# Performance work log

Hardware: AMD Instinct MI355X
Metric: run time of the kernel (lower is better)

## Reference

```python
import jax, jax.numpy as jnp
import numpy as np

N = 100000   # nodes
E = 1600000  # edges (avg degree 16)
G = 64       # graphs in the batch


def setup_inputs() -> dict:
    key = jax.random.key(0)
    ks = jax.random.split(key, 12)
    x = jax.random.normal(ks[0], (N, 1), jnp.float32)
    src = jax.random.randint(ks[1], (E,), 0, N)
    dst = jax.random.randint(ks[2], (E,), 0, N)
    batch = jnp.sort(jax.random.randint(ks[3], (N,), 0, G))
    def glorot(k, shape):
        fan_in, fan_out = shape
        lim = (6.0 / (fan_in + fan_out)) ** 0.5
        return jax.random.uniform(k, shape, jnp.float32, -lim, lim)
    return {
        "x": x, "src": src, "dst": dst, "batch": batch,
        "W1": glorot(ks[4], (1, 100)),   "b1": jnp.zeros((100,), jnp.float32),
        "W2": glorot(ks[5], (100, 200)), "b2": jnp.zeros((200,), jnp.float32),
        "Wl1": glorot(ks[6], (200, 100)), "bl1": jnp.zeros((100,), jnp.float32),
        "Wl2": glorot(ks[7], (100, 1)),   "bl2": jnp.zeros((1,), jnp.float32),
    }


def gcn_layer(x, W, b, src, dst, n_nodes):
    """PyG GCNConv: linear, then sym-normalized aggregation with self-loops, then bias."""
    h = x @ W                                   # [N, out]
    deg = jax.ops.segment_sum(jnp.ones_like(src, dtype=h.dtype), dst,
                              num_segments=n_nodes) + 1.0  # +1 for self-loop
    dinv = jax.lax.rsqrt(deg)                   # [N]
    norm = dinv[src] * dinv[dst]                # [E]
    agg = jax.ops.segment_sum(h[src] * norm[:, None], dst, num_segments=n_nodes)
    agg = agg + h * (dinv * dinv)[:, None]      # self-loop message
    return agg + b


def reference(x, src, dst, batch, W1, b1, W2, b2, Wl1, bl1, Wl2, bl2):
    n = x.shape[0]
    h = jax.nn.silu(gcn_layer(x, W1, b1, src, dst, n))       # [N,100]
    h = jax.nn.silu(gcn_layer(h, W2, b2, src, dst, n))       # [N,200]
    counts = jax.ops.segment_sum(jnp.ones((n,), h.dtype), batch, num_segments=G)
    pooled = jax.ops.segment_sum(h, batch, num_segments=G) / jnp.maximum(counts, 1.0)[:, None]
    h = jax.nn.silu(pooled @ Wl1 + bl1)                      # [G,100]
    out = h @ Wl2 + bl2                                      # [G,1]
    return out.squeeze(-1)                                   # [G]
```

## Files before the change

### kernel.cpp

```cpp
#include <hip/hip_runtime.h>
#include <math.h>

#define F1 100
#define F2 200
#define KM 16
#define BW_LOG 9
#define BW 512

__device__ __forceinline__ float siluf(float v) {
    return v / (1.0f + expf(-v));
}
__device__ __forceinline__ float silu_fast(float v) {
    return __fdividef(v, 1.0f + __expf(-v));
}

#define PREP_BLOCKS 16
__global__ __launch_bounds__(256) void k_prep(
    const int* __restrict__ batch, int N, int G, int nbk,
    int* __restrict__ starts, int* __restrict__ counts,
    double* __restrict__ pooled, int* __restrict__ bcnt, unsigned* __restrict__ amax) {
    int t = threadIdx.x;
    int b = blockIdx.x;
    for (int idx = b * 256 + t; idx < G * F2; idx += PREP_BLOCKS * 256)
        pooled[idx] = 0.0;
    if (b == 1) {
        for (int i = t; i < nbk; i += 256) bcnt[i] = 0;
        if (t == 0) *amax = 0u;
    }
    if (b == 0) {
        if (t <= G) {
            int lo = 0, hi = N;
            while (lo < hi) {
                int mid = (lo + hi) >> 1;
                if (batch[mid] < t) lo = mid + 1; else hi = mid;
            }
            starts[t] = lo;
        }
        __syncthreads();
        if (t < G) counts[t] = starts[t + 1] - starts[t];
    }
}

__global__ __launch_bounds__(256) void k_bucket_count(const int* __restrict__ dst, int E,
                                                      int nbk, int* __restrict__ gcnt) {
    extern __shared__ int cnt[];
    for (int i = threadIdx.x; i < nbk; i += 256) cnt[i] = 0;
    __syncthreads();
    for (int e = blockIdx.x * 256 + threadIdx.x; e < E; e += gridDim.x * 256)
        atomicAdd(&cnt[dst[e] >> BW_LOG], 1);
    __syncthreads();
    for (int i = threadIdx.x; i < nbk; i += 256)
        if (cnt[i]) atomicAdd(&gcnt[i], cnt[i]);
}

__global__ __launch_bounds__(256) void k_bucket_scan(const int* __restrict__ gcnt, int nbk, int E,
                                                     int* __restrict__ base, int* __restrict__ cursor) {
    __shared__ int sh[256];
    int t = threadIdx.x;
    int v = (t < nbk) ? gcnt[t] : 0;
    sh[t] = v;
    __syncthreads();
    for (int ofs = 1; ofs < 256; ofs <<= 1) {
        int u = (t >= ofs) ? sh[t - ofs] : 0;
        __syncthreads();
        sh[t] += u;
        __syncthreads();
    }
    if (t < nbk) { int ex = sh[t] - v; base[t] = ex; cursor[t] = ex; }
    if (t == 0) base[nbk] = E;
}

#define CROUND 4096
#define CEPT 16
__global__ __launch_bounds__(256) void k_bucket_scatter(
    const int* __restrict__ src, const int* __restrict__ dst, int E, int nbk,
    int* __restrict__ gcursor, unsigned long long* __restrict__ pairs) {
    __shared__ int cnt[256];
    __shared__ int scanb[256];
    __shared__ int startx[256];
    __shared__ int cur[256];
    __shared__ int gbase[256];
    __shared__ unsigned long long stage[CROUND];
    int tid = threadIdx.x;
    for (long long r0 = (long long)blockIdx.x * CROUND; r0 < E; r0 += (long long)gridDim.x * CROUND) {
        cnt[tid] = 0;
        __syncthreads();
        int ss[CEPT], dd[CEPT], bb[CEPT];
        bool va[CEPT];
        #pragma unroll
        for (int j = 0; j < CEPT; ++j) {
            long long e = r0 + j * 256 + tid;
            va[j] = (e < E);
            if (va[j]) {
                ss[j] = src[e]; dd[j] = dst[e]; bb[j] = dd[j] >> BW_LOG;
                atomicAdd(&cnt[bb[j]], 1);
            }
        }
        __syncthreads();
        scanb[tid] = cnt[tid];
        __syncthreads();
        for (int ofs = 1; ofs < 256; ofs <<= 1) {
            int u = (tid >= ofs) ? scanb[tid - ofs] : 0;
            __syncthreads();
            scanb[tid] += u;
            __syncthreads();
        }
        int ex = scanb[tid] - cnt[tid];
        startx[tid] = ex;
        cur[tid] = ex;
        if (tid < nbk && cnt[tid] > 0) gbase[tid] = atomicAdd(&gcursor[tid], cnt[tid]);
        __syncthreads();
        int total = scanb[255];
        #pragma unroll
        for (int j = 0; j < CEPT; ++j) {
            if (va[j]) {
                int slot = atomicAdd(&cur[bb[j]], 1);
                stage[slot] = ((unsigned long long)(unsigned)dd[j] << 32) | (unsigned)ss[j];
            }
        }
        __syncthreads();
        for (int i = tid; i < total; i += 256) {
            unsigned long long p = stage[i];
            int b = (int)(p >> 32) >> BW_LOG;
            pairs[gbase[b] + (i - startx[b])] = p;
        }
        __syncthreads();
    }
}

__global__ __launch_bounds__(512) void k_bucket_degoff(
    const unsigned long long* __restrict__ pairs, const int* __restrict__ bbase,
    const float* __restrict__ x, int N,
    float* __restrict__ dinv, float* __restrict__ y, int* __restrict__ off) {
    __shared__ int dl[BW];
    __shared__ int sc[BW];
    int b = blockIdx.x;
    int t = threadIdx.x;
    dl[t] = 0;
    __syncthreads();
    int beg = bbase[b], end = bbase[b + 1];
    for (int i = beg + t; i < end; i += 512)
        atomicAdd(&dl[(int)(pairs[i] >> 32) & (BW - 1)], 1);
    __syncthreads();
    int node = (b << BW_LOG) + t;
    int dg = dl[t];
    if (node < N) {
        float d = 1.0f / sqrtf((float)dg + 1.0f);
        dinv[node] = d;
        y[node] = x[node] * d;
    }
    sc[t] = dg;
    __syncthreads();
    for (int ofs = 1; ofs < BW; ofs <<= 1) {
        int u = (t >= ofs) ? sc[t - ofs] : 0;
        __syncthreads();
        sc[t] += u;
        __syncthreads();
    }
    if (node < N) off[node] = beg + sc[t] - dg;
    if (node == N - 1) off[N] = beg + sc[t];
}

__global__ __launch_bounds__(512) void k_bucket_fill(
    const unsigned long long* __restrict__ pairs, const int* __restrict__ bbase,
    const int* __restrict__ off, const float* __restrict__ y, const float* __restrict__ dinv,
    int N, int* __restrict__ nbr, float2* __restrict__ aggxd, unsigned* __restrict__ amax) {
    __shared__ int offl[BW];
    __shared__ int cur[BW];
    __shared__ float agg[BW];
    int b = blockIdx.x;
    int t = threadIdx.x;
    int node0 = b << BW_LOG;
    int node = node0 + t;
    offl[t] = (node < N) ? off[node] : 0;
    cur[t] = 0;
    agg[t] = 0.0f;
    __syncthreads();
    int beg = bbase[b], end = bbase[b + 1];
    for (int i = beg + t; i < end; i += 512) {
        unsigned long long p = pairs[i];
        int s = (int)(p & 0xffffffffu);
        int d = (int)(p >> 32);
        int l = d & (BW - 1);
        int pos = atomicAdd(&cur[l], 1);
        nbr[offl[l] + pos] = s;
        atomicAdd(&agg[l], y[s]);
    }
    __syncthreads();
    float av = 0.0f;
    if (node < N) {
        float dn = dinv[node];
        float a = dn * (agg[t] + y[node]);
        aggxd[node] = make_float2(a, dn);
        av = fabsf(a);
    }
    __syncthreads();
    agg[t] = av;
    __syncthreads();
    for (int ofs = 256; ofs > 0; ofs >>= 1) {
        if (t < ofs) agg[t] = fmaxf(agg[t], agg[t + ofs]);
        __syncthreads();
    }
    if (t == 0) atomicMax(amax, __float_as_uint(agg[0]));
}

__global__ __launch_bounds__(64) void k_fit_coef(
    const float* __restrict__ W1, const float* __restrict__ b1,
    const unsigned* __restrict__ amax_bits,
    double* __restrict__ cl , float* __restrict__ scal ) {
    int j = blockIdx.x;
    int i = threadIdx.x;
    float A = __uint_as_float(*amax_bits);
    if (!(A > 0.0f)) A = 1.0f;
    A *= 1.000001f;
    if (j == 0 && i == 0) { scal[0] = A; scal[1] = 1.0f / A; }
    const double PI = 3.14159265358979323846;
    double th = (i + 0.5) * (PI / 64.0);
    double xx = cos(th);
    double w = (double)W1[j] * (double)A;
    double u = w * xx + (double)b1[j];
    double f = u / (1.0 + exp(-u));
    double acc[KM];
    {
        double c0 = 1.0, c1 = xx;
        acc[0] = f;
        acc[1] = f * xx;
        #pragma unroll
        for (int k = 2; k < KM; ++k) {
            double c2 = 2.0 * xx * c1 - c0;
            acc[k] = f * c2;
            c0 = c1; c1 = c2;
        }
    }
    #pragma unroll
    for (int k = 0; k < KM; ++k) {
        double v = acc[k];
        for (int ofs = 32; ofs > 0; ofs >>= 1)
            v += __shfl_down(v, ofs);
        if (i == 0) cl[k * F1 + j] = v * ((k == 0 ? 1.0 : 2.0) / 64.0);
    }
}

__global__ __launch_bounds__(256) void k_fit_fold(
    const double* __restrict__ cl, const float* __restrict__ W2,
    float* __restrict__ Dmat ) {
    __shared__ double scl[KM * F1];
    int tid = threadIdx.x;
    for (int idx = tid; idx < KM * F1; idx += 256) scl[idx] = cl[idx];
    __syncthreads();
    int idx = blockIdx.x * 256 + tid;
    if (idx >= KM * F2) return;
    int k = idx / F2, m = idx % F2;
    double s = 0.0;
    #pragma unroll 4
    for (int j = 0; j < F1; ++j)
        s += scl[k * F1 + j] * (double)W2[j * F2 + m];
    Dmat[idx] = (float)s;
}

__global__ __launch_bounds__(256) void k_moments(
    const int* __restrict__ off, const int* __restrict__ nbr,
    const float2* __restrict__ aggxd, const float* __restrict__ scal,
    int N, float* __restrict__ Mrow ) {
    int n = blockIdx.x * 256 + threadIdx.x;
    if (n >= N) return;
    float invA = scal[1];
    float2 sd = aggxd[n];
    float d0 = sd.y;
    float m[KM];
    {
        float xa = sd.x * invA;
        float w = d0 * d0;
        float tx = xa + xa;
        float c0 = 1.0f, c1 = xa;
        m[0] = w; m[1] = w * xa;
        #pragma unroll
        for (int k = 2; k < KM; ++k) {
            float c2 = fmaf(tx, c1, -c0);
            m[k] = w * c2;
            c0 = c1; c1 = c2;
        }
    }
    int beg = off[n], end = off[n + 1];
    for (int e = beg; e < end; ++e) {
        int s = nbr[e];
        float2 q = aggxd[s];
        float w = q.y * d0;
        float xa = q.x * invA;
        float tx = xa + xa;
        float c0 = 1.0f, c1 = xa;
        m[0] += w;
        m[1] = fmaf(w, c1, m[1]);
        #pragma unroll
        for (int k = 2; k < KM; ++k) {
            float c2 = fmaf(tx, c1, -c0);
            m[k] = fmaf(w, c2, m[k]);
            c0 = c1; c1 = c2;
        }
    }
    float4* out4 = (float4*)(Mrow + (size_t)n * KM);
    out4[0] = make_float4(m[0], m[1], m[2], m[3]);
    out4[1] = make_float4(m[4], m[5], m[6], m[7]);
    out4[2] = make_float4(m[8], m[9], m[10], m[11]);
    out4[3] = make_float4(m[12], m[13], m[14], m[15]);
}

#define P6_NODES 32
__global__ __launch_bounds__(256) void k_h2_pool6(
    const float* __restrict__ Mrow, const float* __restrict__ Dmat,
    const float* __restrict__ b2, const int* __restrict__ batch,
    int N, double* __restrict__ pooled) {
    __shared__ float sM[P6_NODES][KM];
    __shared__ int sbatch[P6_NODES];
    int tid = threadIdx.x;
    int base = blockIdx.x * P6_NODES;
    if (tid < P6_NODES * 4) {
        int node = tid >> 2, q = tid & 3;
        float4 v = make_float4(0.f, 0.f, 0.f, 0.f);
        if (base + node < N)
            v = ((const float4*)(Mrow + (size_t)(base + node) * KM))[q];
        ((float4*)&sM[node][0])[q] = v;
    }
    if (tid < P6_NODES) {
        int n = base + tid;
        sbatch[tid] = (n < N) ? batch[n] : -1;
    }
    int m = tid;
    bool act = (m < F2);
    float4 d4[KM / 4];
    float bb = 0.0f;
    if (act) {
        #pragma unroll
        for (int k = 0; k < KM / 4; ++k) {
            d4[k].x = Dmat[(4 * k + 0) * F2 + m];
            d4[k].y = Dmat[(4 * k + 1) * F2 + m];
            d4[k].z = Dmat[(4 * k + 2) * F2 + m];
            d4[k].w = Dmat[(4 * k + 3) * F2 + m];
        }
        bb = b2[m];
    }
    __syncthreads();
    double pl = 0.0;
    int gcur = -1;
    int nlim = min(P6_NODES, N - base);
    int i = 0;
    for (; i + 1 < nlim; i += 2) {
        float preA, preB;
        {
            const float4* mA = (const float4*)&sM[i][0];
            const float4* mB = (const float4*)&sM[i + 1][0];
            float4 a0 = mA[0], a1 = mA[1], a2 = mA[2], a3 = mA[3];
            float4 c0 = mB[0], c1 = mB[1], c2 = mB[2], c3 = mB[3];
            float p0 = bb, p1 = 0.f, p2 = 0.f, p3 = 0.f;
            float q0 = bb, q1 = 0.f, q2 = 0.f, q3 = 0.f;
            p0 = fmaf(a0.x, d4[0].x, p0); q0 = fmaf(c0.x, d4[0].x, q0);
            p1 = fmaf(a0.y, d4[0].y, p1); q1 = fmaf(c0.y, d4[0].y, q1);
            p2 = fmaf(a0.z, d4[0].z, p2); q2 = fmaf(c0.z, d4[0].z, q2);
            p3 = fmaf(a0.w, d4[0].w, p3); q3 = fmaf(c0.w, d4[0].w, q3);
            p0 = fmaf(a1.x, d4[1].x, p0); q0 = fmaf(c1.x, d4[1].x, q0);
            p1 = fmaf(a1.y, d4[1].y, p1); q1 = fmaf(c1.y, d4[1].y, q1);
            p2 = fmaf(a1.z, d4[1].z, p2); q2 = fmaf(c1.z, d4[1].z, q2);
            p3 = fmaf(a1.w, d4[1].w, p3); q3 = fmaf(c1.w, d4[1].w, q3);
            p0 = fmaf(a2.x, d4[2].x, p0); q0 = fmaf(c2.x, d4[2].x, q0);
            p1 = fmaf(a2.y, d4[2].y, p1); q1 = fmaf(c2.y, d4[2].y, q1);
            p2 = fmaf(a2.z, d4[2].z, p2); q2 = fmaf(c2.z, d4[2].z, q2);
            p3 = fmaf(a2.w, d4[2].w, p3); q3 = fmaf(c2.w, d4[2].w, q3);
            p0 = fmaf(a3.x, d4[3].x, p0); q0 = fmaf(c3.x, d4[3].x, q0);
            p1 = fmaf(a3.y, d4[3].y, p1); q1 = fmaf(c3.y, d4[3].y, q1);
            p2 = fmaf(a3.z, d4[3].z, p2); q2 = fmaf(c3.z, d4[3].z, q2);
            p3 = fmaf(a3.w, d4[3].w, p3); q3 = fmaf(c3.w, d4[3].w, q3);
            preA = (p0 + p1) + (p2 + p3);
            preB = (q0 + q1) + (q2 + q3);
        }
        float hA = silu_fast(preA);
        float hB = silu_fast(preB);
        int g = sbatch[i];
        if (g != gcur) {
            if (gcur >= 0 && act) atomicAdd(&pooled[(size_t)gcur * F2 + m], pl);
            pl = 0.0;
            gcur = g;
        }
        if (act) pl += (double)hA;
        g = sbatch[i + 1];
        if (g != gcur) {
            if (gcur >= 0 && act) atomicAdd(&pooled[(size_t)gcur * F2 + m], pl);
            pl = 0.0;
            gcur = g;
        }
        if (act) pl += (double)hB;
    }
    if (i < nlim) {
        const float4* m4 = (const float4*)&sM[i][0];
        float4 a0 = m4[0], a1 = m4[1], a2 = m4[2], a3 = m4[3];
        float p0 = bb, p1 = 0.f, p2 = 0.f, p3 = 0.f;
        p0 = fmaf(a0.x, d4[0].x, p0); p1 = fmaf(a0.y, d4[0].y, p1);
        p2 = fmaf(a0.z, d4[0].z, p2); p3 = fmaf(a0.w, d4[0].w, p3);
        p0 = fmaf(a1.x, d4[1].x, p0); p1 = fmaf(a1.y, d4[1].y, p1);
        p2 = fmaf(a1.z, d4[1].z, p2); p3 = fmaf(a1.w, d4[1].w, p3);
        p0 = fmaf(a2.x, d4[2].x, p0); p1 = fmaf(a2.y, d4[2].y, p1);
        p2 = fmaf(a2.z, d4[2].z, p2); p3 = fmaf(a2.w, d4[2].w, p3);
        p0 = fmaf(a3.x, d4[3].x, p0); p1 = fmaf(a3.y, d4[3].y, p1);
        p2 = fmaf(a3.z, d4[3].z, p2); p3 = fmaf(a3.w, d4[3].w, p3);
        float pre = (p0 + p1) + (p2 + p3);
        int g = sbatch[i];
        if (g != gcur) {
            if (gcur >= 0 && act) atomicAdd(&pooled[(size_t)gcur * F2 + m], pl);
            pl = 0.0;
            gcur = g;
        }
        if (act) pl += (double)silu_fast(pre);
    }
    if (gcur >= 0 && act) atomicAdd(&pooled[(size_t)gcur * F2 + m], pl);
}

#define SCHUNK 2048
__global__ __launch_bounds__(256) void k_scan_partial(const int* __restrict__ deg, int N,
                                                      int* __restrict__ partials) {
    __shared__ int red[256];
    int base = blockIdx.x * SCHUNK;
    int s = 0;
    for (int i = threadIdx.x; i < SCHUNK; i += 256) {
        int idx = base + i;
        if (idx < N) s += deg[idx];
    }
    red[threadIdx.x] = s;
    __syncthreads();
    for (int ofs = 128; ofs > 0; ofs >>= 1) {
        if (threadIdx.x < ofs) red[threadIdx.x] += red[threadIdx.x + ofs];
        __syncthreads();
    }
    if (threadIdx.x == 0) partials[blockIdx.x] = red[0];
}
__global__ __launch_bounds__(1024) void k_scan_blocks(int* __restrict__ partials, int nb) {
    __shared__ int sh[1024];
    int t = threadIdx.x;
    int v = (t < nb) ? partials[t] : 0;
    sh[t] = v;
    __syncthreads();
    for (int ofs = 1; ofs < 1024; ofs <<= 1) {
        int u = (t >= ofs) ? sh[t - ofs] : 0;
        __syncthreads();
        sh[t] += u;
        __syncthreads();
    }
    if (t < nb) partials[t] = sh[t] - v;
}
__global__ __launch_bounds__(256) void k_scan_final(const int* __restrict__ deg, int N,
                                                    const int* __restrict__ partials,
                                                    int* __restrict__ off) {
    __shared__ int sh[256];
    int base = blockIdx.x * SCHUNK;
    int i0 = base + threadIdx.x * 8;
    int v[8];
    int s = 0;
    #pragma unroll
    for (int j = 0; j < 8; ++j) {
        int idx = i0 + j;
        v[j] = (idx < N) ? deg[idx] : 0;
        s += v[j];
    }
    int mine = s;
    sh[threadIdx.x] = s;
    __syncthreads();
    for (int ofs = 1; ofs < 256; ofs <<= 1) {
        int u = (threadIdx.x >= ofs) ? sh[threadIdx.x - ofs] : 0;
        __syncthreads();
        sh[threadIdx.x] += u;
        __syncthreads();
    }
    int run = partials[blockIdx.x] + sh[threadIdx.x] - mine;
    #pragma unroll
    for (int j = 0; j < 8; ++j) {
        int idx = i0 + j;
        if (idx < N) { off[idx] = run; run += v[j]; }
    }
    if (N >= i0 && N <= i0 + 8) off[N] = run;
}
__global__ void k_count_deg(const int* __restrict__ dst, int E, int* __restrict__ deg) {
    int i = blockIdx.x * blockDim.x + threadIdx.x;
    if (i < E) atomicAdd(&deg[dst[i]], 1);
}
__global__ void k_dinv_self(const int* __restrict__ deg, const float* __restrict__ x, int N,
                            float* __restrict__ dinv, float* __restrict__ aggx) {
    int i = blockIdx.x * blockDim.x + threadIdx.x;
    if (i < N) {
        float d = 1.0f / sqrtf((float)deg[i] + 1.0f);
        dinv[i] = d;
        aggx[i] = x[i] * d * d;
    }
}
__global__ void k_fill_agg(const int* __restrict__ src, const int* __restrict__ dst, int E,
                           const int* __restrict__ off, int* __restrict__ cursor,
                           int* __restrict__ nbr,
                           const float* __restrict__ x, const float* __restrict__ dinv,
                           float* __restrict__ aggx) {
    int e = blockIdx.x * blockDim.x + threadIdx.x;
    if (e < E) {
        int s = src[e], d = dst[e];
        int p = atomicAdd(&cursor[d], 1);
        nbr[off[d] + p] = s;
        atomicAdd(&aggx[d], x[s] * dinv[s] * dinv[d]);
    }
}
__global__ __launch_bounds__(256) void k_aggh(
    const int* __restrict__ off, const int* __restrict__ nbr,
    const float* __restrict__ aggx, const float* __restrict__ dinv,
    const float* __restrict__ W1, const float* __restrict__ b1,
    int N, float* __restrict__ aggh) {
    int wave = threadIdx.x >> 6;
    int lane = threadIdx.x & 63;
    int n = blockIdx.x * 4 + wave;
    if (n >= N) return;
    int ja = lane, jb = lane + 64;
    float w1a = (ja < F1) ? W1[ja] : 0.0f;
    float b1a = (ja < F1) ? b1[ja] : 0.0f;
    float w1b = (jb < F1) ? W1[jb] : 0.0f;
    float b1b = (jb < F1) ? b1[jb] : 0.0f;
    float d0 = dinv[n];
    float a0 = aggx[n];
    float accA = silu_fast(fmaf(a0, w1a, b1a)) * (d0 * d0);
    float accB = silu_fast(fmaf(a0, w1b, b1b)) * (d0 * d0);
    int beg = off[n], end = off[n + 1];
    for (int t = beg; t < end; t += 64) {
        int cnt = min(64, end - t);
        float sa = 0.0f, sw = 0.0f;
        if (lane < cnt) {
            int s = nbr[t + lane];
            sa = aggx[s];
            sw = dinv[s] * d0;
        }
        for (int i = 0; i < cnt; ++i) {
            float ai = __shfl(sa, i);
            float wi = __shfl(sw, i);
            accA = fmaf(wi, silu_fast(fmaf(ai, w1a, b1a)), accA);
            accB = fmaf(wi, silu_fast(fmaf(ai, w1b, b1b)), accB);
        }
    }
    if (ja < F1) aggh[(size_t)n * F1 + ja] = accA;
    if (jb < F1) aggh[(size_t)n * F1 + jb] = accB;
}
#define HP_NODES 20
#define HP_KT 25
__global__ __launch_bounds__(256) void k_h2_pool3(
    const float* __restrict__ aggh, const float* __restrict__ W2, const float* __restrict__ b2,
    const int* __restrict__ batch, int N, double* __restrict__ pooled) {
    __shared__ float smem[HP_KT * F2 + HP_NODES * (F1 + 1)];
    float* sW = smem;
    float* sA = smem + HP_KT * F2;
    float* sOut = smem;
    __shared__ int sbatch[HP_NODES];
    int tid = threadIdx.x;
    int base = blockIdx.x * HP_NODES;
    for (int idx = tid; idx < HP_NODES * (F1 / 4); idx += 256) {
        int i = idx / (F1 / 4), q = idx % (F1 / 4);
        int n = base + i;
        float4 v = make_float4(0.f, 0.f, 0.f, 0.f);
        if (n < N) v = *(const float4*)(aggh + (size_t)n * F1 + q * 4);
        float* dp = &sA[i * (F1 + 1) + q * 4];
        dp[0] = v.x; dp[1] = v.y; dp[2] = v.z; dp[3] = v.w;
    }
    if (tid < HP_NODES) {
        int n = base + tid;
        sbatch[tid] = (n < N) ? batch[n] : -1;
    }
    const int fgrp = tid % 50;
    const int ngrp = tid / 50;
    const int m0 = fgrp * 4;
    const int i0 = ngrp * 4;
    const bool act = (tid < 250);
    float acc[4][4];
    #pragma unroll
    for (int i = 0; i < 4; ++i)
        #pragma unroll
        for (int j = 0; j < 4; ++j) acc[i][j] = 0.0f;
    for (int kt = 0; kt < F1; kt += HP_KT) {
        __syncthreads();
        for (int idx = tid; idx < (HP_KT * F2) / 4; idx += 256)
            ((float4*)sW)[idx] = ((const float4*)(W2 + (size_t)kt * F2))[idx];
        __syncthreads();
        if (act) {
            #pragma unroll
            for (int kk = 0; kk < HP_KT; ++kk) {
                float4 w = *(const float4*)&sW[kk * F2 + m0];
                int k = kt + kk;
                float a0 = sA[(i0 + 0) * (F1 + 1) + k];
                float a1 = sA[(i0 + 1) * (F1 + 1) + k];
                float a2 = sA[(i0 + 2) * (F1 + 1) + k];
                float a3 = sA[(i0 + 3) * (F1 + 1) + k];
                acc[0][0] = fmaf(a0, w.x, acc[0][0]); acc[0][1] = fmaf(a0, w.y, acc[0][1]);
                acc[0][2] = fmaf(a0, w.z, acc[0][2]); acc[0][3] = fmaf(a0, w.w, acc[0][3]);
                acc[1][0] = fmaf(a1, w.x, acc[1][0]); acc[1][1] = fmaf(a1, w.y, acc[1][1]);
                acc[1][2] = fmaf(a1, w.z, acc[1][2]); acc[1][3] = fmaf(a1, w.w, acc[1][3]);
                acc[2][0] = fmaf(a2, w.x, acc[2][0]); acc[2][1] = fmaf(a2, w.y, acc[2][1]);
                acc[2][2] = fmaf(a2, w.z, acc[2][2]); acc[2][3] = fmaf(a2, w.w, acc[2][3]);
                acc[3][0] = fmaf(a3, w.x, acc[3][0]); acc[3][1] = fmaf(a3, w.y, acc[3][1]);
                acc[3][2] = fmaf(a3, w.z, acc[3][2]); acc[3][3] = fmaf(a3, w.w, acc[3][3]);
            }
        }
    }
    __syncthreads();
    if (act) {
        float4 bb = *(const float4*)(b2 + m0);
        #pragma unroll
        for (int i = 0; i < 4; ++i) {
            float4 r;
            r.x = siluf(acc[i][0] + bb.x);
            r.y = siluf(acc[i][1] + bb.y);
            r.z = siluf(acc[i][2] + bb.z);
            r.w = siluf(acc[i][3] + bb.w);
            *(float4*)&sOut[(i0 + i) * F2 + m0] = r;
        }
    }
    __syncthreads();
    if (tid < F2) {
        double pl = 0.0;
        int gcur = -1;
        for (int i = 0; i < HP_NODES; ++i) {
            int n = base + i;
            if (n >= N) break;
            int g = sbatch[i];
            if (g != gcur) {
                if (gcur >= 0) atomicAdd(&pooled[(size_t)gcur * F2 + tid], pl);
                pl = 0.0;
                gcur = g;
            }
            pl += (double)sOut[i * F2 + tid];
        }
        if (gcur >= 0) atomicAdd(&pooled[(size_t)gcur * F2 + tid], pl);
    }
}

__global__ __launch_bounds__(256) void k_head(
    const double* __restrict__ pooled, const int* __restrict__ counts,
    const float* __restrict__ Wl1, const float* __restrict__ bl1,
    const float* __restrict__ Wl2, const float* __restrict__ bl2,
    float* __restrict__ out) {
    int g = blockIdx.x;
    int tid = threadIdx.x;
    __shared__ double sp[F2];
    __shared__ double red[256];
    double icnt = 1.0 / (double)max(counts[g], 1);
    for (int m = tid; m < F2; m += 256) sp[m] = pooled[(size_t)g * F2 + m] * icnt;
    __syncthreads();
    double part = 0.0;
    if (tid < 100) {
        double acc = (double)bl1[tid];
        #pragma unroll 4
        for (int m = 0; m < F2; ++m) acc += sp[m] * (double)Wl1[m * 100 + tid];
        double t1 = acc / (1.0 + exp(-acc));
        part = t1 * (double)Wl2[tid];
    }
    red[tid] = part;
    __syncthreads();
    for (int s = 128; s > 0; s >>= 1) {
        if (tid < s) red[tid] += red[tid + s];
        __syncthreads();
    }
    if (tid == 0) out[g] = (float)(red[0] + (double)bl2[0]);
}

extern "C" void kernel_launch(void* const* d_in, const int* in_sizes, int n_in,
                              void* d_out, int out_size, void* d_ws, size_t ws_size,
                              hipStream_t stream)
{
    const float* x   = (const float*)d_in[0];
    const int*   src = (const int*)d_in[1];
    const int*   dst = (const int*)d_in[2];
    const int*   batch = (const int*)d_in[3];
    const float* W1  = (const float*)d_in[4];
    const float* b1  = (const float*)d_in[5];
    const float* W2  = (const float*)d_in[6];
    const float* b2  = (const float*)d_in[7];
    const float* Wl1 = (const float*)d_in[8];
    const float* bl1 = (const float*)d_in[9];
    const float* Wl2 = (const float*)d_in[10];
    const float* bl2 = (const float*)d_in[11];
    int N = in_sizes[0];
    int E = in_sizes[1];
    int G = out_size;
    float* out = (float*)d_out;

    char* ws = (char*)d_ws;
    size_t o = 0;
    auto alloc = [&](size_t bytes) -> void* {
        o = (o + 255) & ~(size_t)255;
        void* p = ws + o;
        o += bytes;
        return p;
    };
    int nscan = (N + SCHUNK - 1) / SCHUNK;
    int nbk = (N + BW - 1) / BW;
    int*    deg    = (int*)alloc((size_t)N * 4);
    int*    cursor = (int*)alloc((size_t)N * 4);
    int*    off    = (int*)alloc((size_t)(N + 1) * 4);
    int*    nbr    = (int*)alloc((size_t)E * 4);
    float*  dinv   = (float*)alloc((size_t)N * 4);
    float*  aggx   = (float*)alloc((size_t)N * 4);
    float*  yv     = (float*)alloc((size_t)N * 4);
    float*  aggh   = (float*)alloc((size_t)N * F1 * 4);
    double* pooled = (double*)alloc((size_t)G * F2 * 8);
    int*    counts = (int*)alloc((size_t)G * 4);
    int*    starts = (int*)alloc((size_t)(G + 1) * 4);
    int*    partials = (int*)alloc((size_t)nscan * 4);
    int*    bcnt   = (int*)alloc((size_t)nbk * 4);
    int*    bbase  = (int*)alloc((size_t)(nbk + 1) * 4);
    int*    bcur   = (int*)alloc((size_t)nbk * 4);
    float2* aggxd  = (float2*)alloc((size_t)N * 8);
    float*  Mrow   = (float*)alloc((size_t)N * KM * 4);
    float*  Dmat   = (float*)alloc((size_t)KM * F2 * 4);
    double* clbuf  = (double*)alloc((size_t)KM * F1 * 8);
    float*  scal   = (float*)alloc(2 * 4);
    unsigned* amaxb = (unsigned*)alloc(4);
    o = (o + 255) & ~(size_t)255;
    unsigned long long* pairs = (unsigned long long*)(ws + o);
    bool use_bucket = (o + (size_t)E * 8) <= ws_size;

    int tE = (E + 255) / 256;
    int tN = (N + 255) / 256;

    if (use_bucket) {
        k_prep<<<PREP_BLOCKS, 256, 0, stream>>>(batch, N, G, nbk, starts, counts, pooled, bcnt, amaxb);
        k_bucket_count<<<240, 256, nbk * 4, stream>>>(dst, E, nbk, bcnt);
        k_bucket_scan<<<1, 256, 0, stream>>>(bcnt, nbk, E, bbase, bcur);
        k_bucket_scatter<<<240, 256, 0, stream>>>(src, dst, E, nbk, bcur, pairs);
        k_bucket_degoff<<<nbk, 512, 0, stream>>>(pairs, bbase, x, N, dinv, yv, off);
        k_bucket_fill<<<nbk, 512, 0, stream>>>(pairs, bbase, off, yv, dinv, N, nbr, aggxd, amaxb);
        k_fit_coef<<<F1, 64, 0, stream>>>(W1, b1, amaxb, clbuf, scal);
        k_fit_fold<<<(KM * F2 + 255) / 256, 256, 0, stream>>>(clbuf, W2, Dmat);
        k_moments<<<(N + 255) / 256, 256, 0, stream>>>(off, nbr, aggxd, scal, N, Mrow);
        k_h2_pool6<<<(N + P6_NODES - 1) / P6_NODES, 256, 0, stream>>>(Mrow, Dmat, b2, batch, N, pooled);
    } else {
        k_prep<<<PREP_BLOCKS, 256, 0, stream>>>(batch, N, G, nbk, starts, counts, pooled, bcnt, amaxb);
        hipMemsetAsync(deg, 0, (size_t)N * 4, stream);
        hipMemsetAsync(cursor, 0, (size_t)N * 4, stream);
        k_count_deg<<<tE, 256, 0, stream>>>(dst, E, deg);
        k_dinv_self<<<tN, 256, 0, stream>>>(deg, x, N, dinv, aggx);
        k_scan_partial<<<nscan, 256, 0, stream>>>(deg, N, partials);
        k_scan_blocks<<<1, 1024, 0, stream>>>(partials, nscan);
        k_scan_final<<<nscan, 256, 0, stream>>>(deg, N, partials, off);
        k_fill_agg<<<tE, 256, 0, stream>>>(src, dst, E, off, cursor, nbr, x, dinv, aggx);
        k_aggh<<<(N + 3) / 4, 256, 0, stream>>>(off, nbr, aggx, dinv, W1, b1, N, aggh);
        k_h2_pool3<<<(N + HP_NODES - 1) / HP_NODES, 256, 0, stream>>>(aggh, W2, b2, batch, N, pooled);
    }
    k_head<<<G, 256, 0, stream>>>(pooled, counts, Wl1, bl1, Wl2, bl2, out);
}
```

Measured before the change: 154.5 us.

## Fuse Chebyshev moment accumulation into the pooling kernel with 8-lane edge split

Merges the per-node moment kernel into the h2 pooling kernel. Each node's edge list is now split across 8 lanes, and the partial moments are combined with a shuffle reduction before being written straight to shared memory. This removes the Mrow global write and re-read and one kernel launch, and it spreads the irregular per-node edge loop over more threads. In exchange, the degree-scaling factor is applied after the reduction, and each thread now holds 16 accumulators alongside the pooling registers, which may raise register pressure and lower occupancy.

Measured after the change: 144.7 us. 1.07x faster.

```diff
diff --git a/kernel.cpp b/kernel.cpp
--- a/kernel.cpp
+++ b/kernel.cpp
@@ -258,70 +258,17 @@
     Dmat[idx] = (float)s;
 }
 
-__global__ __launch_bounds__(256) void k_moments(
+#define P7_NODES 32
+__global__ __launch_bounds__(256) void k_h2_pool7(
     const int* __restrict__ off, const int* __restrict__ nbr,
     const float2* __restrict__ aggxd, const float* __restrict__ scal,
-    int N, float* __restrict__ Mrow ) {
-    int n = blockIdx.x * 256 + threadIdx.x;
-    if (n >= N) return;
-    float invA = scal[1];
-    float2 sd = aggxd[n];
-    float d0 = sd.y;
-    float m[KM];
-    {
-        float xa = sd.x * invA;
-        float w = d0 * d0;
-        float tx = xa + xa;
-        float c0 = 1.0f, c1 = xa;
-        m[0] = w; m[1] = w * xa;
-        #pragma unroll
-        for (int k = 2; k < KM; ++k) {
-            float c2 = fmaf(tx, c1, -c0);
-            m[k] = w * c2;
-            c0 = c1; c1 = c2;
-        }
-    }
-    int beg = off[n], end = off[n + 1];
-    for (int e = beg; e < end; ++e) {
-        int s = nbr[e];
-        float2 q = aggxd[s];
-        float w = q.y * d0;
-        float xa = q.x * invA;
-        float tx = xa + xa;
-        float c0 = 1.0f, c1 = xa;
-        m[0] += w;
-        m[1] = fmaf(w, c1, m[1]);
-        #pragma unroll
-        for (int k = 2; k < KM; ++k) {
-            float c2 = fmaf(tx, c1, -c0);
-            m[k] = fmaf(w, c2, m[k]);
-            c0 = c1; c1 = c2;
-        }
-    }
-    float4* out4 = (float4*)(Mrow + (size_t)n * KM);
-    out4[0] = make_float4(m[0], m[1], m[2], m[3]);
-    out4[1] = make_float4(m[4], m[5], m[6], m[7]);
-    out4[2] = make_float4(m[8], m[9], m[10], m[11]);
-    out4[3] = make_float4(m[12], m[13], m[14], m[15]);
-}
-
-#define P6_NODES 32
-__global__ __launch_bounds__(256) void k_h2_pool6(
-    const float* __restrict__ Mrow, const float* __restrict__ Dmat,
-    const float* __restrict__ b2, const int* __restrict__ batch,
-    int N, double* __restrict__ pooled) {
-    __shared__ float sM[P6_NODES][KM];
-    __shared__ int sbatch[P6_NODES];
+    const float* __restrict__ Dmat, const float* __restrict__ b2,
+    const int* __restrict__ batch, int N, double* __restrict__ pooled) {
+    __shared__ float sM[P7_NODES][KM];
+    __shared__ int sbatch[P7_NODES];
     int tid = threadIdx.x;
-    int base = blockIdx.x * P6_NODES;
-    if (tid < P6_NODES * 4) {
-        int node = tid >> 2, q = tid & 3;
-        float4 v = make_float4(0.f, 0.f, 0.f, 0.f);
-        if (base + node < N)
-            v = ((const float4*)(Mrow + (size_t)(base + node) * KM))[q];
-        ((float4*)&sM[node][0])[q] = v;
-    }
-    if (tid < P6_NODES) {
+    int base = blockIdx.x * P7_NODES;
+    if (tid < P7_NODES) {
         int n = base + tid;
         sbatch[tid] = (n < N) ? batch[n] : -1;
     }
@@ -339,10 +286,60 @@
         }
         bb = b2[m];
     }
+    {
+        int g = tid >> 3;
+        int l = tid & 7;
+        int node = base + g;
+        float invA = scal[1];
+        float u[KM];
+        #pragma unroll
+        for (int k = 0; k < KM; ++k) u[k] = 0.0f;
+        if (node < N) {
+            int beg = off[node], end = off[node + 1];
+            for (int e = beg + l; e < end; e += 8) {
+                int s = nbr[e];
+                float2 q = aggxd[s];
+                float w = q.y;
+                float xa = q.x * invA;
+                float tx = xa + xa;
+                float c0 = 1.0f, c1 = xa;
+                u[0] += w;
+                u[1] = fmaf(w, c1, u[1]);
+                #pragma unroll
+                for (int k = 2; k < KM; ++k) {
+                    float c2 = fmaf(tx, c1, -c0);
+                    u[k] = fmaf(w, c2, u[k]);
+                    c0 = c1; c1 = c2;
+                }
+            }
+        }
+        #pragma unroll
+        for (int k = 0; k < KM; ++k) {
+            u[k] += __shfl_down(u[k], 4, 8);
+            u[k] += __shfl_down(u[k], 2, 8);
+            u[k] += __shfl_down(u[k], 1, 8);
+        }
+        if (l == 0 && node < N) {
+            float2 sd = aggxd[node];
+            float d0 = sd.y;
+            float d00 = d0 * d0;
+            float xa = sd.x * invA;
+            float tx = xa + xa;
+            float c0 = 1.0f, c1 = xa;
+            sM[g][0] = fmaf(d0, u[0], d00);
+            sM[g][1] = fmaf(d0, u[1], d00 * xa);
+            #pragma unroll
+            for (int k = 2; k < KM; ++k) {
+                float c2 = fmaf(tx, c1, -c0);
+                sM[g][k] = fmaf(d0, u[k], d00 * c2);
+                c0 = c1; c1 = c2;
+            }
+        }
+    }
     __syncthreads();
     double pl = 0.0;
     int gcur = -1;
-    int nlim = min(P6_NODES, N - base);
+    int nlim = min(P7_NODES, N - base);
     int i = 0;
     for (; i + 1 < nlim; i += 2) {
         float preA, preB;
@@ -706,7 +703,6 @@
     int*    bbase  = (int*)alloc((size_t)(nbk + 1) * 4);
     int*    bcur   = (int*)alloc((size_t)nbk * 4);
     float2* aggxd  = (float2*)alloc((size_t)N * 8);
-    float*  Mrow   = (float*)alloc((size_t)N * KM * 4);
     float*  Dmat   = (float*)alloc((size_t)KM * F2 * 4);
     double* clbuf  = (double*)alloc((size_t)KM * F1 * 8);
     float*  scal   = (float*)alloc(2 * 4);
@@ -727,8 +723,8 @@
         k_bucket_fill<<<nbk, 512, 0, stream>>>(pairs, bbase, off, yv, dinv, N, nbr, aggxd, amaxb);
         k_fit_coef<<<F1, 64, 0, stream>>>(W1, b1, amaxb, clbuf, scal);
         k_fit_fold<<<(KM * F2 + 255) / 256, 256, 0, stream>>>(clbuf, W2, Dmat);
-        k_moments<<<(N + 255) / 256, 256, 0, stream>>>(off, nbr, aggxd, scal, N, Mrow);
-        k_h2_pool6<<<(N + P6_NODES - 1) / P6_NODES, 256, 0, stream>>>(Mrow, Dmat, b2, batch, N, pooled);
+        k_h2_pool7<<<(N + P7_NODES - 1) / P7_NODES, 256, 0, stream>>>(
+            off, nbr, aggxd, scal, Dmat, b2, batch, N, pooled);
     } else {
         k_prep<<<PREP_BLOCKS, 256, 0, stream>>>(batch, N, G, nbk, starts, counts, pooled, bcnt, amaxb);
         hipMemsetAsync(deg, 0, (size_t)N * 4, stream);
```
